# Optimization experiments

Measured on AMD Instinct MI355X. Metric: run time of the kernel, lower is better.

Reference implementation:

```python
import jax, jax.numpy as jnp
import numpy as np

N, E, F, H, R, NB, G, C = 100000, 500000, 128, 64, 16, 30, 1000, 10


def setup_inputs() -> dict:
    key = jax.random.key(0)
    ks = jax.random.split(key, 12)
    s = 0.05
    x = jax.random.normal(ks[0], (N, F), jnp.float32)
    edge_index = jax.random.randint(ks[1], (2, E), 0, N, dtype=jnp.int32)
    edge_norm = jax.random.uniform(ks[2], (E,), jnp.float32)
    edge_type = jax.random.randint(ks[3], (E,), 0, R, dtype=jnp.int32)
    seq_lengths = jnp.full((G,), N // G, dtype=jnp.int32)  # 1000 graphs x 100 nodes
    return dict(
        x=x, edge_index=edge_index, edge_norm=edge_norm, edge_type=edge_type,
        seq_lengths=seq_lengths, avec=0,
        w1_rel=jax.random.normal(ks[4], (F, H), jnp.float32) * s,
        w1_root=jax.random.normal(ks[5], (F, H), jnp.float32) * s,
        b1=jnp.zeros((H,), jnp.float32),
        bases=jax.random.normal(ks[6], (NB, H, H), jnp.float32) * s,
        comp=jax.random.normal(ks[7], (R, NB), jnp.float32) * s,
        w2_root=jax.random.normal(ks[8], (H, H), jnp.float32) * s,
        b2=jnp.zeros((H,), jnp.float32),
        lin_w=jax.random.normal(ks[9], (2 * (F + H), H), jnp.float32) * s,
        lin_b=jnp.zeros((H,), jnp.float32),
        fc_w=jax.random.normal(ks[10], (H, C), jnp.float32) * s,
        fc_b=jnp.zeros((C,), jnp.float32),
    )


def reference(x, edge_index, edge_norm, edge_type, seq_lengths, avec,
              w1_rel, w1_root, b1, bases, comp, w2_root, b2,
              lin_w, lin_b, fc_w, fc_b):
    src, dst = edge_index[0], edge_index[1]

    # --- GraphConv (PyG): out_i = W_rel @ sum_{j->i} w_ji x_j + W_root x_i + b
    msg = x[src] * edge_norm[:, None]                       # [E, F]
    agg = jax.ops.segment_sum(msg, dst, num_segments=N)     # [N, F]
    h = agg @ w1_rel + x @ w1_root + b1                     # [N, H]

    # --- RGCNConv with basis decomposition, mean aggregation per relation
    W = jnp.einsum('rb,bio->rio', comp, bases)              # [R, H, H]
    hs = h[src]                                             # [E, H]
    out = h @ w2_root + b2                                  # root transform + bias
    for r in range(R):  # small fixed relation count
        m = (edge_type == r).astype(h.dtype)                # [E]
        s_r = jax.ops.segment_sum(hs * m[:, None], dst, num_segments=N)
        c_r = jax.ops.segment_sum(m, dst, num_segments=N)
        out = out + (s_r / jnp.maximum(c_r, 1.0)[:, None]) @ W[r]

    feats = jnp.concatenate([x, out], axis=-1)              # [N, F+H]

    # --- ragged per-graph sum & max pooling (replaces the Python loop)
    bounds = jnp.cumsum(seq_lengths)
    gid = jnp.searchsorted(bounds, jnp.arange(N), side='right')  # [N] graph ids
    gsum = jax.ops.segment_sum(feats, gid, num_segments=G)       # [G, F+H]
    gmax = jax.ops.segment_max(feats, gid, num_segments=G)       # [G, F+H]

    hidden = jax.nn.relu(jnp.concatenate([gsum, gmax], -1) @ lin_w + lin_b)
    # dropout is identity at inference
    logits = hidden @ fc_w + fc_b                           # [G, C]
    if avec:
        return logits
    return jax.nn.log_softmax(logits, -1)
```

## Files before the change

kernel.cpp:

```cpp
#include <hip/hip_runtime.h>
#include <hip/hip_bf16.h>

#define NN 100000
#define NE 500000
#define FD 128
#define HD 64
#define RR 16
#define NBASE 30
#define GG 1000
#define CC 10
#define NGROUP 6250
#define NBLK ((NE + 255) / 256)


typedef __attribute__((ext_vector_type(8))) short bf16x8;
typedef __attribute__((ext_vector_type(4))) float f32x4;

__device__ inline unsigned short f2b(float x) {
  __hip_bfloat16 b = __float2bfloat16(x);
  return *reinterpret_cast<unsigned short*>(&b);
}
__device__ inline float b2f(unsigned short u) {
  return __uint_as_float(((unsigned)u) << 16);
}
__device__ inline unsigned pk2(float a, float b) {
  return (unsigned)f2b(a) | ((unsigned)f2b(b) << 16);
}

__global__ void k_prep(const float* comp, const float* bases, const float* w_root,
                       const float* w_rel, const float* w2, unsigned short* Wt,
                       unsigned short* wcat2, unsigned short* w2t) {
  int bx = blockIdx.x;
  if (bx < 256) {
    int idx = bx * 256 + threadIdx.x;
    int r = idx >> 12, kj = idx & 4095;
    int k = kj >> 6, n = kj & 63;
    float acc = 0.0f;
    for (int b = 0; b < NBASE; ++b)
      acc += comp[r * NBASE + b] * bases[b * 4096 + kj];
    int sk = (k & 15) * 4 + (k >> 4);
    Wt[(r << 12) + n * 64 + sk] = f2b(acc);
  } else {
    int idx = (bx - 256) * 256 + threadIdx.x;
    if (idx < 16384) {
      int n = idx >> 7, k = idx & 127;
      float v = (n < 64) ? w_root[k * 64 + n] : w_rel[k * 64 + (n - 64)];
      int nt = n >> 4, m = n & 15;
      int s = k >> 5, q = (k >> 3) & 3, j = k & 7;
      wcat2[(((nt * 4 + s) * 64) + q * 16 + m) * 8 + j] = f2b(v);
    } else if (idx < 16384 + 4096) {
      int i2 = idx - 16384;
      int n = i2 >> 6, k = i2 & 63;
      int sk = (k & 15) * 4 + (k >> 4);
      w2t[n * 64 + sk] = f2b(w2[k * 64 + n]);
    }
  }
}

__global__ __launch_bounds__(256) void k_proj_mfma(const float* x, const unsigned short* wcat2,
                                                   const float* b1, unsigned short* hroot_bf,
                                                   unsigned short* xw_bf) {
  __shared__ unsigned short wsh[16384];
  int wv = threadIdx.x >> 6, l = threadIdx.x & 63, m = l & 15, q = l >> 4;
  int g = blockIdx.x * 4 + wv;
  int gc = (g < NGROUP) ? g : (NGROUP - 1);
  size_t n0 = (size_t)gc * 16;
  const float* xr = x + (n0 + m) * FD + q * 8;
  float4 xv[8];
#pragma unroll
  for (int s = 0; s < 4; ++s) {
    xv[2 * s] = *reinterpret_cast<const float4*>(xr + s * 32);
    xv[2 * s + 1] = *reinterpret_cast<const float4*>(xr + s * 32 + 4);
  }
  {
    const uint4* wsrc = reinterpret_cast<const uint4*>(wcat2);
    uint4* wdst = reinterpret_cast<uint4*>(wsh);
#pragma unroll
    for (int r = 0; r < 8; ++r)
      wdst[r * 256 + threadIdx.x] = wsrc[r * 256 + threadIdx.x];
  }
  __syncthreads();
  if (g >= NGROUP) return;
  bf16x8 afr[4];
#pragma unroll
  for (int s = 0; s < 4; ++s) {
    float4 xa = xv[2 * s], xb = xv[2 * s + 1];
    bf16x8 a;
    a[0] = (short)f2b(xa.x); a[1] = (short)f2b(xa.y);
    a[2] = (short)f2b(xa.z); a[3] = (short)f2b(xa.w);
    a[4] = (short)f2b(xb.x); a[5] = (short)f2b(xb.y);
    a[6] = (short)f2b(xb.z); a[7] = (short)f2b(xb.w);
    afr[s] = a;
  }
  f32x4 acc[8];
#pragma unroll
  for (int nt = 0; nt < 8; ++nt) acc[nt] = (f32x4){0, 0, 0, 0};
#pragma unroll
  for (int s = 0; s < 4; ++s) {
#pragma unroll
    for (int nt = 0; nt < 8; ++nt) {
      bf16x8 b = *reinterpret_cast<const bf16x8*>(wsh + (size_t)((nt * 4 + s) * 64 + l) * 8);
      acc[nt] = __builtin_amdgcn_mfma_f32_16x16x32_bf16(afr[s], b, acc[nt], 0, 0, 0);
    }
  }
  float bv[4];
#pragma unroll
  for (int nt = 0; nt < 4; ++nt) bv[nt] = b1[nt * 16 + m];
#pragma unroll
  for (int i = 0; i < 4; ++i) {
    size_t row = (n0 + q * 4 + i) * 64 + m * 4;
    uint2 oh, ox;
    oh.x = pk2(acc[0][i] + bv[0], acc[1][i] + bv[1]);
    oh.y = pk2(acc[2][i] + bv[2], acc[3][i] + bv[3]);
    ox.x = pk2(acc[4][i], acc[5][i]);
    ox.y = pk2(acc[6][i], acc[7][i]);
    *reinterpret_cast<uint2*>(hroot_bf + row) = oh;
    *reinterpret_cast<uint2*>(xw_bf + row) = ox;
  }
}

__global__ void k_hists(const int* ei, const int* etype, int* bch, int* hist2) {
  __shared__ int lh[RR];
  if (threadIdx.x < RR) lh[threadIdx.x] = 0;
  __syncthreads();
  int e = blockIdx.x * 256 + threadIdx.x;
  if (e < NE) {
    int t = etype[e];
    atomicAdd(&lh[t], 1);
    atomicAdd(&hist2[ei[NE + e] * RR + t], 1);
  }
  __syncthreads();
  if (threadIdx.x < RR) bch[blockIdx.x * RR + threadIdx.x] = lh[threadIdx.x];
}

__device__ inline int block_scan_incl(int v, int* ps, int t) {
  ps[t] = v;
  __syncthreads();
  for (int off = 1; off < 256; off <<= 1) {
    int u = (t >= off) ? ps[t - off] : 0;
    __syncthreads();
    ps[t] += u;
    __syncthreads();
  }
  return ps[t];
}

__global__ void k_scanA(const int* hist2, int* bsum) {
  __shared__ int red[256];
  int t = threadIdx.x;
  red[t] = hist2[blockIdx.x * 256 + t];
  __syncthreads();
  for (int s = 128; s; s >>= 1) {
    if (t < s) red[t] += red[t + s];
    __syncthreads();
  }
  if (t == 0) bsum[blockIdx.x] = red[0];
}

__global__ void k_scanB(int* bsum) {
  int t = threadIdx.x;
  int loc[25];
  int s = 0;
  if (t < 250) {
    for (int i = 0; i < 25; ++i) { loc[i] = bsum[t * 25 + i]; s += loc[i]; }
  }
  __shared__ int ps[256];
  int incl = block_scan_incl(s, ps, t);
  int base = incl - s;
  if (t < 250) {
    int run = base;
    for (int i = 0; i < 25; ++i) { int tmp = loc[i]; bsum[t * 25 + i] = run; run += tmp; }
  }
}

__global__ void k_scanC(const int* hist2, const int* bsum, int* rowptr2, int* ctr2) {
  int t = threadIdx.x;
  int gid = blockIdx.x * 256 + t;
  int v = hist2[gid];
  __shared__ int ps[256];
  int incl = block_scan_incl(v, ps, t);
  int ex = bsum[blockIdx.x] + incl - v;
  rowptr2[gid] = ex;
  ctr2[gid] = ex | (v << 20);
}

__global__ void k_bscan(const int* bch, const int* seq, int* bbase, int* offs, int* bounds) {
  __shared__ int part[16][17], chunkbase[16][17];
  __shared__ int colbase[16];
  __shared__ int ps[256];
  int t = threadIdx.x;
  int ty = t & 15, ck = t >> 4;
  const int CH = (NBLK + 15) / 16;
  int b0 = ck * CH, b1 = min(b0 + CH, NBLK);
  int s = 0;
  for (int b = b0; b < b1; ++b) s += bch[b * 16 + ty];
  part[ck][ty] = s;
  __syncthreads();
  if (t < 16) {
    int run = 0;
    for (int c = 0; c < 16; ++c) { chunkbase[c][t] = run; run += part[c][t]; }
    colbase[t] = run;
  }
  __syncthreads();
  if (t == 0) {
    int run = 0;
    for (int r = 0; r < RR; ++r) { int v = colbase[r]; offs[r] = run; colbase[r] = run; run += v; }
    offs[RR] = run;
  }
  __syncthreads();
  {
    int run = colbase[ty] + chunkbase[ck][ty];
    for (int b = b0; b < b1; ++b) {
      int v = bch[b * 16 + ty];
      bbase[b * 16 + ty] = run;
      run += v;
    }
  }
  int loc[4];
  int ss = 0;
  if (t < 250) {
    for (int i = 0; i < 4; ++i) { loc[i] = seq[t * 4 + i]; ss += loc[i]; }
  }
  int incl = block_scan_incl(ss, ps, t);
  int base = incl - ss;
  if (t < 250) {
    int run = base;
    for (int i = 0; i < 4; ++i) { run += loc[i]; bounds[t * 4 + i] = run; }
  }
}

__global__ void k_sort(const int* ei, const int* etype, const float* enorm,
                       const int* bbase, int* ctr2, uint4* tse, uint2* esen) {
  __shared__ int lcnt[RR];
  if (threadIdx.x < RR) lcnt[threadIdx.x] = 0;
  __syncthreads();
  int e = blockIdx.x * 256 + threadIdx.x;
  if (e >= NE) return;
  int t = etype[e];
  int rank = atomicAdd(&lcnt[t], 1);
  int p = bbase[blockIdx.x * RR + t] + rank;
  int src = ei[e];
  int key = ei[NE + e] * RR + t;
  int old = atomicAdd(&ctr2[key], 1);
  int pos = old & 0xFFFFF;
  int cnt = old >> 20;
  float inv = 1.0f / (float)max(cnt, 1);
  esen[pos] = make_uint2((unsigned)src, __float_as_uint(enorm[e]));
  tse[p] = make_uint4((unsigned)src, __float_as_uint(inv), (unsigned)pos, 0u);
}

__global__ __launch_bounds__(256) void k_gconv_seg(const int* rowptr2, const uint2* esen,
    const unsigned short* xw_bf, const unsigned short* hroot_bf, unsigned short* h_bf) {
  int wv = threadIdx.x >> 6, l = threadIdx.x & 63;
  int c4 = l & 15, eq = l >> 4;
  int dst = blockIdx.x * 4 + wv;
  int lo = rowptr2[dst * RR];
  int hi = (dst == NN - 1) ? NE : rowptr2[(dst + 1) * RR];
  float4 acc = {0.0f, 0.0f, 0.0f, 0.0f};
  for (int base0 = lo; base0 < hi; base0 += 64) {
    int n = min(64, hi - base0);
    int sv = 0;
    float nv = 0.0f;
    if (l < n) {
      uint2 se = esen[base0 + l];
      sv = (int)se.x;
      nv = __uint_as_float(se.y);
    }
    int k4max = (n + 3) >> 2;
    for (int k4 = 0; k4 < k4max; ++k4) {
      int eid = k4 * 4 + eq;
      int s = __shfl(sv, eid);
      float w = __shfl(nv, eid);
      if (eid < n) {
        uint2 v = *reinterpret_cast<const uint2*>(xw_bf + (size_t)s * 64 + c4 * 4);
        acc.x += b2f((unsigned short)(v.x & 0xffffu)) * w;
        acc.y += b2f((unsigned short)(v.x >> 16)) * w;
        acc.z += b2f((unsigned short)(v.y & 0xffffu)) * w;
        acc.w += b2f((unsigned short)(v.y >> 16)) * w;
      }
    }
  }
  acc.x += __shfl_xor(acc.x, 16); acc.y += __shfl_xor(acc.y, 16);
  acc.z += __shfl_xor(acc.z, 16); acc.w += __shfl_xor(acc.w, 16);
  acc.x += __shfl_xor(acc.x, 32); acc.y += __shfl_xor(acc.y, 32);
  acc.z += __shfl_xor(acc.z, 32); acc.w += __shfl_xor(acc.w, 32);
  if (l < 16) {
    uint2 hb = *reinterpret_cast<const uint2*>(hroot_bf + (size_t)dst * 64 + l * 4);
    acc.x += b2f((unsigned short)(hb.x & 0xffffu));
    acc.y += b2f((unsigned short)(hb.x >> 16));
    acc.z += b2f((unsigned short)(hb.y & 0xffffu));
    acc.w += b2f((unsigned short)(hb.y >> 16));
    uint2 o;
    o.x = pk2(acc.x, acc.y);
    o.y = pk2(acc.z, acc.w);
    *reinterpret_cast<uint2*>(h_bf + (size_t)dst * 64 + l * 4) = o;
  }
}

__global__ __launch_bounds__(256) void k_rgcn_y(const uint4* tse, const int* offs,
    const unsigned short* h_bf, const unsigned short* Wt, unsigned short* y_bf) {
  int r = blockIdx.x;
  int lo = offs[r], hi = offs[r + 1];
  int cnt = hi - lo;
  int wv = threadIdx.x >> 6;
  int l = threadIdx.x & 63;
  int m = l & 15, q = l >> 4;
  int ngroups = (cnt + 15) / 16;
  const unsigned short* Wr = Wt + (r << 12);
  bf16x8 bfr[2][4];
#pragma unroll
  for (int s = 0; s < 2; ++s)
#pragma unroll
    for (int nt = 0; nt < 4; ++nt)
      bfr[s][nt] = *reinterpret_cast<const bf16x8*>(Wr + (nt * 16 + m) * 64 + s * 32 + q * 8);

  for (int g = blockIdx.y * 4 + wv; g < ngroups; g += gridDim.y * 4) {
    int base = lo + g * 16;
    int ne = min(16, hi - base);
    int p = base + ((m < ne) ? m : 0);
    uint4 t4 = tse[p];
    int src = (int)t4.x;
    float inv = __uint_as_float(t4.y);
    int pos = (int)t4.z;
    f32x4 acc[4];
#pragma unroll
    for (int nt = 0; nt < 4; ++nt) acc[nt] = (f32x4){0, 0, 0, 0};
    const unsigned short* hrow = h_bf + (size_t)src * 64 + q * 8;
#pragma unroll
    for (int s = 0; s < 2; ++s) {
      bf16x8 afr = *reinterpret_cast<const bf16x8*>(hrow + s * 32);
#pragma unroll
      for (int nt = 0; nt < 4; ++nt)
        acc[nt] = __builtin_amdgcn_mfma_f32_16x16x32_bf16(afr, bfr[s][nt], acc[nt], 0, 0, 0);
    }
#pragma unroll
    for (int i = 0; i < 4; ++i) {
      int row = q * 4 + i;
      float ir = __shfl(inv, row);
      int pr = __shfl(pos, row);
      if (row < ne) {
        uint2 o;
        o.x = pk2(acc[0][i] * ir, acc[1][i] * ir);
        o.y = pk2(acc[2][i] * ir, acc[3][i] * ir);
        *reinterpret_cast<uint2*>(y_bf + (size_t)pr * 64 + m * 4) = o;
      }
    }
  }
}

__global__ __launch_bounds__(256) void k_out(const int* rowptr2, const unsigned short* y_bf,
    const unsigned short* h_bf, const unsigned short* w2t, const float* b2, float* out) {
  __shared__ float ldsC[16][68];
  int wv = threadIdx.x >> 6, l = threadIdx.x & 63;
  int c4 = l & 15, eq = l >> 4;
  size_t d0 = (size_t)blockIdx.x * 16;
  for (int dd = 0; dd < 4; ++dd) {
    int dst = (int)d0 + wv * 4 + dd;
    int lo = rowptr2[dst * RR];
    int hi = (dst == NN - 1) ? NE : rowptr2[(dst + 1) * RR];
    float4 acc = {0.0f, 0.0f, 0.0f, 0.0f};
    for (int row = lo + eq; row < hi; row += 4) {
      uint2 v = *reinterpret_cast<const uint2*>(y_bf + (size_t)row * 64 + c4 * 4);
      acc.x += b2f((unsigned short)(v.x & 0xffffu));
      acc.y += b2f((unsigned short)(v.x >> 16));
      acc.z += b2f((unsigned short)(v.y & 0xffffu));
      acc.w += b2f((unsigned short)(v.y >> 16));
    }
    acc.x += __shfl_xor(acc.x, 16); acc.y += __shfl_xor(acc.y, 16);
    acc.z += __shfl_xor(acc.z, 16); acc.w += __shfl_xor(acc.w, 16);
    acc.x += __shfl_xor(acc.x, 32); acc.y += __shfl_xor(acc.y, 32);
    acc.z += __shfl_xor(acc.z, 32); acc.w += __shfl_xor(acc.w, 32);
    if (l < 16)
      *reinterpret_cast<float4*>(&ldsC[wv * 4 + dd][l * 4]) = acc;
  }
  __syncthreads();
  int m = l & 15, q = l >> 4, nt = wv;
  float bb = b2[nt * 16 + m];
  f32x4 acc;
#pragma unroll
  for (int i = 0; i < 4; ++i) acc[i] = ldsC[q * 4 + i][m * 4 + nt] + bb;
#pragma unroll
  for (int s = 0; s < 2; ++s) {
    bf16x8 a = *reinterpret_cast<const bf16x8*>(h_bf + (d0 + m) * 64 + s * 32 + q * 8);
    bf16x8 b = *reinterpret_cast<const bf16x8*>(w2t + (nt * 16 + m) * 64 + s * 32 + q * 8);
    acc = __builtin_amdgcn_mfma_f32_16x16x32_bf16(a, b, acc, 0, 0, 0);
  }
#pragma unroll
  for (int i = 0; i < 4; ++i)
    out[(d0 + q * 4 + i) * 64 + nt * 16 + m] = acc[i];
}

__global__ __launch_bounds__(256) void k_head(const float* x, const float* outn,
    const int* bounds, const float* lin_w, const float* lin_b,
    const float* fc_w, const float* fc_b, float* dout) {
  __shared__ float4 psum[5][48], pmax[5][48];
  __shared__ float gsum[192], gmax[192];
  __shared__ float part[4][64];
  __shared__ float hid[HD], lg[CC], mred[2];
  int g = blockIdx.x, t = threadIdx.x;
  int lo = (g == 0) ? 0 : bounds[g - 1];
  int hi = bounds[g];
  int nn = hi - lo;
  if (t < 240) {
    int c4 = t % 48, ch = t / 48;
    int a = lo + (nn * ch) / 5, b = lo + (nn * (ch + 1)) / 5;
    float4 s = {0, 0, 0, 0};
    float4 mx = {-3.4e38f, -3.4e38f, -3.4e38f, -3.4e38f};
    const float* bp;
    int stride;
    if (c4 < 32) { bp = x + (size_t)a * FD + c4 * 4; stride = FD; }
    else         { bp = outn + (size_t)a * 64 + (c4 - 32) * 4; stride = 64; }
    int n = a;
    for (; n + 4 <= b; n += 4) {
      float4 v0 = *reinterpret_cast<const float4*>(bp);
      float4 v1 = *reinterpret_cast<const float4*>(bp + stride);
      float4 v2 = *reinterpret_cast<const float4*>(bp + 2 * stride);
      float4 v3 = *reinterpret_cast<const float4*>(bp + 3 * stride);
      bp += 4 * stride;
      s.x += v0.x + v1.x + v2.x + v3.x;
      s.y += v0.y + v1.y + v2.y + v3.y;
      s.z += v0.z + v1.z + v2.z + v3.z;
      s.w += v0.w + v1.w + v2.w + v3.w;
      mx.x = fmaxf(fmaxf(fmaxf(mx.x, v0.x), fmaxf(v1.x, v2.x)), v3.x);
      mx.y = fmaxf(fmaxf(fmaxf(mx.y, v0.y), fmaxf(v1.y, v2.y)), v3.y);
      mx.z = fmaxf(fmaxf(fmaxf(mx.z, v0.z), fmaxf(v1.z, v2.z)), v3.z);
      mx.w = fmaxf(fmaxf(fmaxf(mx.w, v0.w), fmaxf(v1.w, v2.w)), v3.w);
    }
    for (; n < b; ++n) {
      float4 v = *reinterpret_cast<const float4*>(bp);
      bp += stride;
      s.x += v.x; s.y += v.y; s.z += v.z; s.w += v.w;
      mx.x = fmaxf(mx.x, v.x); mx.y = fmaxf(mx.y, v.y);
      mx.z = fmaxf(mx.z, v.z); mx.w = fmaxf(mx.w, v.w);
    }
    psum[ch][c4] = s;
    pmax[ch][c4] = mx;
  }
  __syncthreads();
  if (t < 48) {
    float4 s = psum[0][t], m = pmax[0][t];
#pragma unroll
    for (int ch = 1; ch < 5; ++ch) {
      float4 ps = psum[ch][t], pm = pmax[ch][t];
      s.x += ps.x; s.y += ps.y; s.z += ps.z; s.w += ps.w;
      m.x = fmaxf(m.x, pm.x); m.y = fmaxf(m.y, pm.y);
      m.z = fmaxf(m.z, pm.z); m.w = fmaxf(m.w, pm.w);
    }
    gsum[t * 4 + 0] = s.x; gsum[t * 4 + 1] = s.y;
    gsum[t * 4 + 2] = s.z; gsum[t * 4 + 3] = s.w;
    gmax[t * 4 + 0] = m.x; gmax[t * 4 + 1] = m.y;
    gmax[t * 4 + 2] = m.z; gmax[t * 4 + 3] = m.w;
  }
  __syncthreads();
  {
    int o = t & 63, pp = t >> 6;
    float a = 0.0f;
    int k0 = pp * 96;
    for (int k = k0; k < k0 + 96; ++k) {
      float gv = (k < 192) ? gsum[k] : gmax[k - 192];
      a += gv * lin_w[k * 64 + o];
    }
    part[pp][o] = a;
  }
  __syncthreads();
  if (t < HD) {
    float a = lin_b[t] + part[0][t] + part[1][t] + part[2][t] + part[3][t];
    hid[t] = fmaxf(a, 0.0f);
  }
  __syncthreads();
  if (t < CC) {
    float a = fc_b[t];
    for (int k = 0; k < HD; ++k) a += hid[k] * fc_w[k * CC + t];
    lg[t] = a;
  }
  __syncthreads();
  if (t == 0) {
    float mm = lg[0];
#pragma unroll
    for (int i = 1; i < CC; ++i) mm = fmaxf(mm, lg[i]);
    float se = 0.0f;
#pragma unroll
    for (int i = 0; i < CC; ++i) se += __expf(lg[i] - mm);
    mred[0] = mm;
    mred[1] = __logf(se);
  }
  __syncthreads();
  if (t < CC) dout[g * CC + t] = lg[t] - mred[0] - mred[1];
}

extern "C" void kernel_launch(void* const* d_in, const int* in_sizes, int n_in,
                              void* d_out, int out_size, void* d_ws, size_t ws_size,
                              hipStream_t stream) {
  const float* x     = (const float*)d_in[0];
  const int* ei      = (const int*)d_in[1];
  const float* enorm = (const float*)d_in[2];
  const int* etype   = (const int*)d_in[3];
  const int* seq     = (const int*)d_in[4];
  const float* w1_rel  = (const float*)d_in[6];
  const float* w1_root = (const float*)d_in[7];
  const float* b1      = (const float*)d_in[8];
  const float* bases   = (const float*)d_in[9];
  const float* comp    = (const float*)d_in[10];
  const float* w2      = (const float*)d_in[11];
  const float* b2      = (const float*)d_in[12];
  const float* lin_w   = (const float*)d_in[13];
  const float* lin_b   = (const float*)d_in[14];
  const float* fc_w    = (const float*)d_in[15];
  const float* fc_b    = (const float*)d_in[16];
  float* dout = (float*)d_out;

  char* p = (char*)d_ws;
  unsigned short* hroot_bf = (unsigned short*)p; p += (size_t)NN * 64 * 2;
  unsigned short* xw_bf    = (unsigned short*)p; p += (size_t)NN * 64 * 2;
  float* out  = (float*)p;  p += (size_t)NN * 64 * 4;
  unsigned short* y_bf = (unsigned short*)p; p += (size_t)NE * 64 * 2;
  unsigned short* h_bf = (unsigned short*)p; p += (size_t)NN * 64 * 2;
  unsigned short* Wt   = (unsigned short*)p; p += (size_t)RR * 4096 * 2;
  unsigned short* wcat2 = (unsigned short*)p; p += (size_t)128 * 128 * 2;
  unsigned short* w2t  = (unsigned short*)p; p += (size_t)64 * 64 * 2;
  uint4* tse   = (uint4*)p; p += (size_t)NE * 16;
  uint2* esen  = (uint2*)p; p += (size_t)NE * 8;
  int* hist2   = (int*)p; p += (size_t)NN * RR * 4;
  int* rowptr2 = (int*)p; p += (size_t)NN * RR * 4;
  int* bch     = (int*)p; p += (size_t)NBLK * RR * 4;
  int* bbase   = (int*)p; p += (size_t)NBLK * RR * 4;
  int* bsum    = (int*)p; p += (size_t)NGROUP * 4;
  int* offs    = (int*)p; p += 68;
  int* bounds  = (int*)p; p += (size_t)GG * 4;
  int* ctr2    = (int*)out;

  hipMemsetAsync(hist2, 0, (size_t)NN * RR * 4, stream);

  hipLaunchKernelGGL(k_prep, dim3(256 + 80), dim3(256), 0, stream,
                     comp, bases, w1_root, w1_rel, w2, Wt, wcat2, w2t);
  hipLaunchKernelGGL(k_proj_mfma, dim3((NGROUP + 3) / 4), dim3(256), 0, stream,
                     x, wcat2, b1, hroot_bf, xw_bf);
  hipLaunchKernelGGL(k_hists, dim3(NBLK), dim3(256), 0, stream, ei, etype, bch, hist2);
  hipLaunchKernelGGL(k_scanA, dim3(NGROUP), dim3(256), 0, stream, hist2, bsum);
  hipLaunchKernelGGL(k_scanB, dim3(1), dim3(256), 0, stream, bsum);
  hipLaunchKernelGGL(k_scanC, dim3(NGROUP), dim3(256), 0, stream, hist2, bsum, rowptr2, ctr2);
  hipLaunchKernelGGL(k_bscan, dim3(1), dim3(256), 0, stream, bch, seq, bbase, offs, bounds);
  hipLaunchKernelGGL(k_sort, dim3(NBLK), dim3(256), 0, stream,
                     ei, etype, enorm, bbase, ctr2, tse, esen);
  hipLaunchKernelGGL(k_gconv_seg, dim3(NN / 4), dim3(256), 0, stream,
                     rowptr2, esen, xw_bf, hroot_bf, h_bf);
  hipLaunchKernelGGL(k_rgcn_y, dim3(RR, 128), dim3(256), 0, stream,
                     tse, offs, h_bf, Wt, y_bf);
  hipLaunchKernelGGL(k_out, dim3(NN / 16), dim3(256), 0, stream,
                     rowptr2, y_bf, h_bf, w2t, b2, out);
  hipLaunchKernelGGL(k_head, dim3(GG), dim3(256), 0, stream, x, out, bounds,
                     lin_w, lin_b, fc_w, fc_b, dout);
}
```

Before: 341.1 us.

## Scan per-destination degrees instead of per-(dst,relation) histogram and fold scan kernels

Replaces the 1.6M-entry (dst,relation) exclusive scan with a scan over per-destination degrees (100K entries). Each degree is computed by summing the 16 relation counts. The hist2 memset moves into extra blocks of k_prep, and the tiny block-sum scan is merged into k_bscan, which removes a memset and one kernel launch. k_sort now reads the per-relation count directly from hist2 and does an atomic on a per-destination counter. The intent is to cut scan traffic and launch overhead. The trade-off is that edges within a destination are no longer grouped by relation, which k_out tolerates because it only sums rows.

```diff
diff --git a/kernel.cpp b/kernel.cpp
--- a/kernel.cpp
+++ b/kernel.cpp
@@ -11,6 +11,7 @@
 #define CC 10
 #define NGROUP 6250
 #define NBLK ((NE + 255) / 256)
+#define NDBLK ((NN + 256) / 256)
 
 
 typedef __attribute__((ext_vector_type(8))) short bf16x8;
@@ -29,7 +30,7 @@
 
 __global__ void k_prep(const float* comp, const float* bases, const float* w_root,
                        const float* w_rel, const float* w2, unsigned short* Wt,
-                       unsigned short* wcat2, unsigned short* w2t) {
+                       unsigned short* wcat2, unsigned short* w2t, int* hist2) {
   int bx = blockIdx.x;
   if (bx < 256) {
     int idx = bx * 256 + threadIdx.x;
@@ -40,7 +41,7 @@
       acc += comp[r * NBASE + b] * bases[b * 4096 + kj];
     int sk = (k & 15) * 4 + (k >> 4);
     Wt[(r << 12) + n * 64 + sk] = f2b(acc);
-  } else {
+  } else if (bx < 336) {
     int idx = (bx - 256) * 256 + threadIdx.x;
     if (idx < 16384) {
       int n = idx >> 7, k = idx & 127;
@@ -54,6 +55,10 @@
       int sk = (k & 15) * 4 + (k >> 4);
       w2t[n * 64 + sk] = f2b(w2[k * 64 + n]);
     }
+  } else {
+    int idx = (bx - 336) * 1024 + threadIdx.x * 4;
+    if (idx < NN * RR)
+      *reinterpret_cast<int4*>(hist2 + idx) = make_int4(0, 0, 0, 0);
   }
 }
 
@@ -145,10 +150,18 @@
   return ps[t];
 }
 
+__device__ inline int dst_degree(const int* hist2, int dst) {
+  const int4* hp = reinterpret_cast<const int4*>(hist2 + dst * RR);
+  int4 a = hp[0], b = hp[1], c = hp[2], d = hp[3];
+  return a.x + a.y + a.z + a.w + b.x + b.y + b.z + b.w +
+         c.x + c.y + c.z + c.w + d.x + d.y + d.z + d.w;
+}
+
 __global__ void k_scanA(const int* hist2, int* bsum) {
   __shared__ int red[256];
   int t = threadIdx.x;
-  red[t] = hist2[blockIdx.x * 256 + t];
+  int dst = blockIdx.x * 256 + t;
+  red[t] = (dst < NN) ? dst_degree(hist2, dst) : 0;
   __syncthreads();
   for (int s = 128; s; s >>= 1) {
     if (t < s) red[t] += red[t + s];
@@ -157,38 +170,34 @@
   if (t == 0) bsum[blockIdx.x] = red[0];
 }
 
-__global__ void k_scanB(int* bsum) {
+__global__ void k_scanC(const int* hist2, const int* bsum, int* rowptr_d, int* ctr_d) {
   int t = threadIdx.x;
-  int loc[25];
-  int s = 0;
-  if (t < 250) {
-    for (int i = 0; i < 25; ++i) { loc[i] = bsum[t * 25 + i]; s += loc[i]; }
-  }
-  __shared__ int ps[256];
-  int incl = block_scan_incl(s, ps, t);
-  int base = incl - s;
-  if (t < 250) {
-    int run = base;
-    for (int i = 0; i < 25; ++i) { int tmp = loc[i]; bsum[t * 25 + i] = run; run += tmp; }
-  }
-}
-
-__global__ void k_scanC(const int* hist2, const int* bsum, int* rowptr2, int* ctr2) {
-  int t = threadIdx.x;
-  int gid = blockIdx.x * 256 + t;
-  int v = hist2[gid];
+  int dst = blockIdx.x * 256 + t;
+  int v = (dst < NN) ? dst_degree(hist2, dst) : 0;
   __shared__ int ps[256];
   int incl = block_scan_incl(v, ps, t);
   int ex = bsum[blockIdx.x] + incl - v;
-  rowptr2[gid] = ex;
-  ctr2[gid] = ex | (v << 20);
-}
-
-__global__ void k_bscan(const int* bch, const int* seq, int* bbase, int* offs, int* bounds) {
+  if (dst <= NN) { rowptr_d[dst] = ex; ctr_d[dst] = ex; }
+}
+
+__global__ void k_bscan(const int* bch, const int* seq, int* bsum, int* bbase,
+                        int* offs, int* bounds) {
   __shared__ int part[16][17], chunkbase[16][17];
   __shared__ int colbase[16];
   __shared__ int ps[256];
   int t = threadIdx.x;
+  {
+    int i0 = t * 2, i1 = t * 2 + 1;
+    int l0 = (i0 < NDBLK) ? bsum[i0] : 0;
+    int l1 = (i1 < NDBLK) ? bsum[i1] : 0;
+    int sa = l0 + l1;
+    int incla = block_scan_incl(sa, ps, t);
+    int run = incla - sa;
+    if (i0 < NDBLK) bsum[i0] = run;
+    run += l0;
+    if (i1 < NDBLK) bsum[i1] = run;
+  }
+  __syncthreads();
   int ty = t & 15, ck = t >> 4;
   const int CH = (NBLK + 15) / 16;
   int b0 = ck * CH, b1 = min(b0 + CH, NBLK);
@@ -216,6 +225,7 @@
       run += v;
     }
   }
+  __syncthreads();
   int loc[4];
   int ss = 0;
   if (t < 250) {
@@ -230,7 +240,8 @@
 }
 
 __global__ void k_sort(const int* ei, const int* etype, const float* enorm,
-                       const int* bbase, int* ctr2, uint4* tse, uint2* esen) {
+                       const int* bbase, const int* hist2, int* ctr_d,
+                       uint4* tse, uint2* esen) {
   __shared__ int lcnt[RR];
   if (threadIdx.x < RR) lcnt[threadIdx.x] = 0;
   __syncthreads();
@@ -240,22 +251,21 @@
   int rank = atomicAdd(&lcnt[t], 1);
   int p = bbase[blockIdx.x * RR + t] + rank;
   int src = ei[e];
-  int key = ei[NE + e] * RR + t;
-  int old = atomicAdd(&ctr2[key], 1);
-  int pos = old & 0xFFFFF;
-  int cnt = old >> 20;
+  int dst = ei[NE + e];
+  int cnt = hist2[dst * RR + t];
   float inv = 1.0f / (float)max(cnt, 1);
+  int pos = atomicAdd(&ctr_d[dst], 1);
   esen[pos] = make_uint2((unsigned)src, __float_as_uint(enorm[e]));
   tse[p] = make_uint4((unsigned)src, __float_as_uint(inv), (unsigned)pos, 0u);
 }
 
-__global__ __launch_bounds__(256) void k_gconv_seg(const int* rowptr2, const uint2* esen,
+__global__ __launch_bounds__(256) void k_gconv_seg(const int* rowptr_d, const uint2* esen,
     const unsigned short* xw_bf, const unsigned short* hroot_bf, unsigned short* h_bf) {
   int wv = threadIdx.x >> 6, l = threadIdx.x & 63;
   int c4 = l & 15, eq = l >> 4;
   int dst = blockIdx.x * 4 + wv;
-  int lo = rowptr2[dst * RR];
-  int hi = (dst == NN - 1) ? NE : rowptr2[(dst + 1) * RR];
+  int lo = rowptr_d[dst];
+  int hi = rowptr_d[dst + 1];
   float4 acc = {0.0f, 0.0f, 0.0f, 0.0f};
   for (int base0 = lo; base0 < hi; base0 += 64) {
     int n = min(64, hi - base0);
@@ -348,7 +358,7 @@
   }
 }
 
-__global__ __launch_bounds__(256) void k_out(const int* rowptr2, const unsigned short* y_bf,
+__global__ __launch_bounds__(256) void k_out(const int* rowptr_d, const unsigned short* y_bf,
     const unsigned short* h_bf, const unsigned short* w2t, const float* b2, float* out) {
   __shared__ float ldsC[16][68];
   int wv = threadIdx.x >> 6, l = threadIdx.x & 63;
@@ -356,8 +366,8 @@
   size_t d0 = (size_t)blockIdx.x * 16;
   for (int dd = 0; dd < 4; ++dd) {
     int dst = (int)d0 + wv * 4 + dd;
-    int lo = rowptr2[dst * RR];
-    int hi = (dst == NN - 1) ? NE : rowptr2[(dst + 1) * RR];
+    int lo = rowptr_d[dst];
+    int hi = rowptr_d[dst + 1];
     float4 acc = {0.0f, 0.0f, 0.0f, 0.0f};
     for (int row = lo + eq; row < hi; row += 4) {
       uint2 v = *reinterpret_cast<const uint2*>(y_bf + (size_t)row * 64 + c4 * 4);
@@ -521,33 +531,31 @@
   uint4* tse   = (uint4*)p; p += (size_t)NE * 16;
   uint2* esen  = (uint2*)p; p += (size_t)NE * 8;
   int* hist2   = (int*)p; p += (size_t)NN * RR * 4;
-  int* rowptr2 = (int*)p; p += (size_t)NN * RR * 4;
+  int* rowptr_d = (int*)p; p += (size_t)(NDBLK * 256) * 4;
   int* bch     = (int*)p; p += (size_t)NBLK * RR * 4;
   int* bbase   = (int*)p; p += (size_t)NBLK * RR * 4;
   int* bsum    = (int*)p; p += (size_t)NGROUP * 4;
   int* offs    = (int*)p; p += 68;
   int* bounds  = (int*)p; p += (size_t)GG * 4;
-  int* ctr2    = (int*)out;
-
-  hipMemsetAsync(hist2, 0, (size_t)NN * RR * 4, stream);
-
-  hipLaunchKernelGGL(k_prep, dim3(256 + 80), dim3(256), 0, stream,
-                     comp, bases, w1_root, w1_rel, w2, Wt, wcat2, w2t);
+  int* ctr_d   = (int*)out;
+
+  const int ZBLK = (NN * RR + 1023) / 1024;
+  hipLaunchKernelGGL(k_prep, dim3(336 + ZBLK), dim3(256), 0, stream,
+                     comp, bases, w1_root, w1_rel, w2, Wt, wcat2, w2t, hist2);
   hipLaunchKernelGGL(k_proj_mfma, dim3((NGROUP + 3) / 4), dim3(256), 0, stream,
                      x, wcat2, b1, hroot_bf, xw_bf);
   hipLaunchKernelGGL(k_hists, dim3(NBLK), dim3(256), 0, stream, ei, etype, bch, hist2);
-  hipLaunchKernelGGL(k_scanA, dim3(NGROUP), dim3(256), 0, stream, hist2, bsum);
-  hipLaunchKernelGGL(k_scanB, dim3(1), dim3(256), 0, stream, bsum);
-  hipLaunchKernelGGL(k_scanC, dim3(NGROUP), dim3(256), 0, stream, hist2, bsum, rowptr2, ctr2);
-  hipLaunchKernelGGL(k_bscan, dim3(1), dim3(256), 0, stream, bch, seq, bbase, offs, bounds);
+  hipLaunchKernelGGL(k_scanA, dim3(NDBLK), dim3(256), 0, stream, hist2, bsum);
+  hipLaunchKernelGGL(k_bscan, dim3(1), dim3(256), 0, stream, bch, seq, bsum, bbase, offs, bounds);
+  hipLaunchKernelGGL(k_scanC, dim3(NDBLK), dim3(256), 0, stream, hist2, bsum, rowptr_d, ctr_d);
   hipLaunchKernelGGL(k_sort, dim3(NBLK), dim3(256), 0, stream,
-                     ei, etype, enorm, bbase, ctr2, tse, esen);
+                     ei, etype, enorm, bbase, hist2, ctr_d, tse, esen);
   hipLaunchKernelGGL(k_gconv_seg, dim3(NN / 4), dim3(256), 0, stream,
-                     rowptr2, esen, xw_bf, hroot_bf, h_bf);
+                     rowptr_d, esen, xw_bf, hroot_bf, h_bf);
   hipLaunchKernelGGL(k_rgcn_y, dim3(RR, 128), dim3(256), 0, stream,
                      tse, offs, h_bf, Wt, y_bf);
   hipLaunchKernelGGL(k_out, dim3(NN / 16), dim3(256), 0, stream,
-                     rowptr2, y_bf, h_bf, w2t, b2, out);
+                     rowptr_d, y_bf, h_bf, w2t, b2, out);
   hipLaunchKernelGGL(k_head, dim3(GG), dim3(256), 0, stream, x, out, bounds,
                      lin_w, lin_b, fc_w, fc_b, dout);
 }
```

Measured after the change: 331.1 us. 2.9% less time.
